# Kernel tuning notes

Measured on AMD Instinct MI355X. Metric: run time of the kernel, lower is better.

## Reference

```python
import jax, jax.numpy as jnp
import numpy as np

N_NODES = 50000
N_EDGES = 800000
IN_FEATS = 128
N_HIDDEN = 64
OUT_FEATS = 40
DIM = 8  # pseudo-coordinate dimension
K = 1    # n_kernels


def setup_inputs() -> dict:
    key = jax.random.key(0)
    ks = jax.random.split(key, 12)
    inp = {
        "features": jax.random.normal(ks[0], (N_NODES, IN_FEATS), dtype=jnp.float32),
        "edge_weight": jax.random.normal(ks[1], (N_EDGES, DIM), dtype=jnp.float32),
        "src": jax.random.randint(ks[2], (N_EDGES,), 0, N_NODES),
        "dst": jax.random.randint(ks[3], (N_EDGES,), 0, N_NODES),
        # layer 1 params (fc has no bias in DGL GMMConv; separate additive bias)
        "W1": jax.random.normal(ks[4], (IN_FEATS, K * N_HIDDEN), dtype=jnp.float32) * (1.0 / np.sqrt(IN_FEATS)),
        "b1": jnp.zeros((N_HIDDEN,), dtype=jnp.float32),
        "mu1": jax.random.normal(ks[5], (K, DIM), dtype=jnp.float32) * 0.1,
        "inv_sigma1": jnp.ones((K, DIM), dtype=jnp.float32),
        # layer 2 params
        "W2": jax.random.normal(ks[6], (N_HIDDEN, K * OUT_FEATS), dtype=jnp.float32) * (1.0 / np.sqrt(N_HIDDEN)),
        "b2": jnp.zeros((OUT_FEATS,), dtype=jnp.float32),
        "mu2": jax.random.normal(ks[7], (K, DIM), dtype=jnp.float32) * 0.1,
        "inv_sigma2": jnp.ones((K, DIM), dtype=jnp.float32),
    }
    return inp


def gmm_conv(x, pseudo, src, dst, W, b, mu, inv_sigma, out_feats):
    # x: [N, in], pseudo: [E, DIM], W: [in, K*out]
    h = (x @ W).reshape(-1, K, out_feats)                      # [N, K, out]
    # gaussian mixture weights per edge/kernel: [E, K]
    diff = pseudo[:, None, :] - mu[None, :, :]                 # [E, K, DIM]
    gw = jnp.exp(-0.5 * jnp.sum(diff * diff * (inv_sigma[None] ** 2), axis=-1))
    # gather src feats, weight, sum over kernels: [E, out]
    msg = jnp.einsum("ekf,ek->ef", h[src], gw)
    agg = jax.ops.segment_sum(msg, dst, num_segments=N_NODES)  # [N, out]
    return agg + b


def reference(features, edge_weight, src, dst, W1, b1, mu1, inv_sigma1, W2, b2, mu2, inv_sigma2):
    x = gmm_conv(features, edge_weight, src, dst, W1, b1, mu1, inv_sigma1, N_HIDDEN)
    x = gmm_conv(x, edge_weight, src, dst, W2, b2, mu2, inv_sigma2, OUT_FEATS)
    return jax.nn.log_softmax(x, axis=1)
```

## Files before the change

### kernel.cpp

```cpp
#include <hip/hip_runtime.h>
#include <hip/hip_fp16.h>
#include <math.h>

#define N_NODES 50000
#define N_EDGES 800000
#define IN_FEATS 128
#define N_HIDDEN 64
#define OUT_FEATS 40
#define DIM 8
#define GT_TILES ((N_NODES + 63) / 64)
#define FILL_BLOCKS (N_EDGES / 256)
#define SCAN_NB ((N_NODES + 255) / 256)

typedef _Float16 half8 __attribute__((ext_vector_type(8)));
typedef float floatx4 __attribute__((ext_vector_type(4)));

__device__ __forceinline__ int wave_incl_scan(int x, int lane) {
#pragma unroll
    for (int off = 1; off < 64; off <<= 1) {
        int v = __shfl_up(x, off, 64);
        if (lane >= off) x += v;
    }
    return x;
}

__global__ __launch_bounds__(256) void hist_kernel(const int* __restrict__ dst,
                                                   int* __restrict__ counts,
                                                   unsigned short* __restrict__ rank) {
    int i = blockIdx.x * 256 + threadIdx.x;
    if (i * 4 >= N_EDGES) return;
    int4 d = ((const int4*)dst)[i];
    ushort4 r;
    r.x = (unsigned short)atomicAdd(&counts[d.x], 1);
    r.y = (unsigned short)atomicAdd(&counts[d.y], 1);
    r.z = (unsigned short)atomicAdd(&counts[d.z], 1);
    r.w = (unsigned short)atomicAdd(&counts[d.w], 1);
    ((ushort4*)rank)[i] = r;
}

__global__ __launch_bounds__(256) void scan_partial_kernel(const int* __restrict__ counts,
                                                           int* __restrict__ offsets,
                                                           int* __restrict__ partials) {
    const int tid = threadIdx.x, bid = blockIdx.x;
    const int i = bid * 256 + tid;
    const int lane = tid & 63, wid = tid >> 6;
    int x = (i < N_NODES) ? counts[i] : 0;
    int incl = wave_incl_scan(x, lane);
    __shared__ int wsum[4];
    if (lane == 63) wsum[wid] = incl;
    __syncthreads();
    int base = 0;
#pragma unroll
    for (int w = 0; w < 4; ++w)
        if (w < wid) base += wsum[w];
    if (i < N_NODES) offsets[i] = base + incl - x;
    if (tid == 255) partials[bid] = base + incl;
}

__global__ __launch_bounds__(256) void scan_base_kernel(int* __restrict__ partials) {
    const int tid = threadIdx.x;
    const int lane = tid & 63, wid = tid >> 6;
    int x = (tid < SCAN_NB) ? partials[tid] : 0;
    int incl = wave_incl_scan(x, lane);
    __shared__ int wsum[4];
    if (lane == 63) wsum[wid] = incl;
    __syncthreads();
    int base = 0;
#pragma unroll
    for (int w = 0; w < 4; ++w)
        if (w < wid) base += wsum[w];
    if (tid < SCAN_NB) partials[tid] = base + incl - x;
}

__global__ __launch_bounds__(256) void scan_add_kernel(int* __restrict__ offsets,
                                                       const int* __restrict__ partials) {
    const int i = blockIdx.x * 256 + threadIdx.x;
    if (i < N_NODES) offsets[i] += partials[blockIdx.x];
    if (i == N_NODES) offsets[N_NODES] = N_EDGES;
}

__global__ __launch_bounds__(256) void fillgemm_kernel(
    const float* __restrict__ features, const float* __restrict__ W1,
    const int* __restrict__ src, const int* __restrict__ dst,
    const float* __restrict__ ew,
    const float* __restrict__ mu1, const float* __restrict__ is1,
    const float* __restrict__ mu2, const float* __restrict__ is2,
    const int* __restrict__ offsets, const unsigned short* __restrict__ rank,
    int2* __restrict__ csr, __half* __restrict__ h1)
{
    const int tid = threadIdx.x;
    __shared__ __align__(16) __half WT[64][136];

    if (blockIdx.x >= GT_TILES) {
        int e = (blockIdx.x - GT_TILES) * 256 + tid;
        int sN = src[e];
        int dN = dst[e];
        unsigned short rk = rank[e];
        const float4* ew4 = (const float4*)(ew + (size_t)e * DIM);
        float4 wa = ew4[0], wb = ew4[1];
        float v[8] = {wa.x, wa.y, wa.z, wa.w, wb.x, wb.y, wb.z, wb.w};
        float s1 = 0.f, s2 = 0.f;
#pragma unroll
        for (int d = 0; d < DIM; ++d) {
            float d1 = v[d] - mu1[d]; float a1 = is1[d];
            float d2 = v[d] - mu2[d]; float a2 = is2[d];
            s1 += d1 * d1 * a1 * a1;
            s2 += d2 * d2 * a2 * a2;
        }
        __half2 g = __floats2half2_rn(expf(-0.5f * s1), expf(-0.5f * s2));
        int2 rec;
        rec.x = sN;
        rec.y = *reinterpret_cast<int*>(&g);
        int pos = offsets[dN] + rk;
        __builtin_nontemporal_store(*reinterpret_cast<long long*>(&rec),
                                    reinterpret_cast<long long*>(&csr[pos]));
        return;
    }

    int nodeBase = blockIdx.x * 64;
    for (int rep = 0; rep < 32; ++rep) {
        int idx = tid + rep * 256;
        int k = idx >> 6, n = idx & 63;
        WT[n][k] = __float2half(W1[idx]);
    }
    __syncthreads();

    int lane = tid & 63, w = tid >> 6;
    int m = lane & 15, quad = lane >> 4;
    int row = nodeBase + w * 16 + m;
    int rowc = (row < N_NODES) ? row : (N_NODES - 1);
    const float* fr = features + (size_t)rowc * IN_FEATS;

    floatx4 acc0 = {0.f,0.f,0.f,0.f}, acc1 = acc0, acc2 = acc0, acc3 = acc0;
#pragma unroll
    for (int kc = 0; kc < 4; ++kc) {
        float4 fa = *(const float4*)(fr + kc * 32 + quad * 8);
        float4 fb = *(const float4*)(fr + kc * 32 + quad * 8 + 4);
        union { half8 v; __half2 h2[4]; } A;
        A.h2[0] = __floats2half2_rn(fa.x, fa.y);
        A.h2[1] = __floats2half2_rn(fa.z, fa.w);
        A.h2[2] = __floats2half2_rn(fb.x, fb.y);
        A.h2[3] = __floats2half2_rn(fb.z, fb.w);
        half8 b0 = *(const half8*)&WT[ 0 + m][kc * 32 + quad * 8];
        half8 b1 = *(const half8*)&WT[16 + m][kc * 32 + quad * 8];
        half8 b2 = *(const half8*)&WT[32 + m][kc * 32 + quad * 8];
        half8 b3 = *(const half8*)&WT[48 + m][kc * 32 + quad * 8];
        acc0 = __builtin_amdgcn_mfma_f32_16x16x32_f16(A.v, b0, acc0, 0, 0, 0);
        acc1 = __builtin_amdgcn_mfma_f32_16x16x32_f16(A.v, b1, acc1, 0, 0, 0);
        acc2 = __builtin_amdgcn_mfma_f32_16x16x32_f16(A.v, b2, acc2, 0, 0, 0);
        acc3 = __builtin_amdgcn_mfma_f32_16x16x32_f16(A.v, b3, acc3, 0, 0, 0);
    }
    int nodeRow = nodeBase + w * 16 + quad * 4;
#pragma unroll
    for (int r = 0; r < 4; ++r) {
        int n = nodeRow + r;
        if (n < N_NODES) {
            size_t base = (size_t)n * N_HIDDEN + m;
            h1[base +  0] = __float2half(acc0[r]);
            h1[base + 16] = __float2half(acc1[r]);
            h1[base + 32] = __float2half(acc2[r]);
            h1[base + 48] = __float2half(acc3[r]);
        }
    }
}

__global__ __launch_bounds__(256) void agg1_gemm2_kernel(const __half* __restrict__ h,
                                                         const int* __restrict__ offsets,
                                                         const int2* __restrict__ csr,
                                                         const float* __restrict__ b,
                                                         const float* __restrict__ W2,
                                                         __half* __restrict__ h2) {
    __shared__ float xs[8][64];
    const unsigned* h32 = (const unsigned*)h;
    const int tid = threadIdx.x;
    const int w = tid >> 6, lane = tid & 63;
    const int hf = lane >> 5, p = lane & 31;
    const int ln = w * 2 + hf;
    const int n = blockIdx.x * 8 + ln;
    int beg = offsets[n], end = offsets[n + 1];

    float ax = 0.f, ay = 0.f;
    for (int j = beg; j < end; j += 8) {
        int j0 = j + 0, j1 = j + 1, j2 = j + 2, j3 = j + 3;
        int j4 = j + 4, j5 = j + 5, j6 = j + 6, j7 = j + 7;
        int e1 = end - 1;
        int2 r0 = csr[(j0 < end) ? j0 : e1];
        int2 r1 = csr[(j1 < end) ? j1 : e1];
        int2 r2 = csr[(j2 < end) ? j2 : e1];
        int2 r3 = csr[(j3 < end) ? j3 : e1];
        int2 r4 = csr[(j4 < end) ? j4 : e1];
        int2 r5 = csr[(j5 < end) ? j5 : e1];
        int2 r6 = csr[(j6 < end) ? j6 : e1];
        int2 r7 = csr[(j7 < end) ? j7 : e1];
        unsigned v0 = h32[(size_t)r0.x * 32 + p];
        unsigned v1 = h32[(size_t)r1.x * 32 + p];
        unsigned v2 = h32[(size_t)r2.x * 32 + p];
        unsigned v3 = h32[(size_t)r3.x * 32 + p];
        unsigned v4 = h32[(size_t)r4.x * 32 + p];
        unsigned v5 = h32[(size_t)r5.x * 32 + p];
        unsigned v6 = h32[(size_t)r6.x * 32 + p];
        unsigned v7 = h32[(size_t)r7.x * 32 + p];
        float g0 = (j0 < end) ? __low2float(*reinterpret_cast<__half2*>(&r0.y)) : 0.f;
        float g1 = (j1 < end) ? __low2float(*reinterpret_cast<__half2*>(&r1.y)) : 0.f;
        float g2 = (j2 < end) ? __low2float(*reinterpret_cast<__half2*>(&r2.y)) : 0.f;
        float g3 = (j3 < end) ? __low2float(*reinterpret_cast<__half2*>(&r3.y)) : 0.f;
        float g4 = (j4 < end) ? __low2float(*reinterpret_cast<__half2*>(&r4.y)) : 0.f;
        float g5 = (j5 < end) ? __low2float(*reinterpret_cast<__half2*>(&r5.y)) : 0.f;
        float g6 = (j6 < end) ? __low2float(*reinterpret_cast<__half2*>(&r6.y)) : 0.f;
        float g7 = (j7 < end) ? __low2float(*reinterpret_cast<__half2*>(&r7.y)) : 0.f;
        float2 f0 = __half22float2(*reinterpret_cast<__half2*>(&v0));
        float2 f1 = __half22float2(*reinterpret_cast<__half2*>(&v1));
        float2 f2 = __half22float2(*reinterpret_cast<__half2*>(&v2));
        float2 f3 = __half22float2(*reinterpret_cast<__half2*>(&v3));
        float2 f4 = __half22float2(*reinterpret_cast<__half2*>(&v4));
        float2 f5 = __half22float2(*reinterpret_cast<__half2*>(&v5));
        float2 f6 = __half22float2(*reinterpret_cast<__half2*>(&v6));
        float2 f7 = __half22float2(*reinterpret_cast<__half2*>(&v7));
        ax += f0.x * g0; ay += f0.y * g0;
        ax += f1.x * g1; ay += f1.y * g1;
        ax += f2.x * g2; ay += f2.y * g2;
        ax += f3.x * g3; ay += f3.y * g3;
        ax += f4.x * g4; ay += f4.y * g4;
        ax += f5.x * g5; ay += f5.y * g5;
        ax += f6.x * g6; ay += f6.y * g6;
        ax += f7.x * g7; ay += f7.y * g7;
    }
    float2 bb = *(const float2*)&b[2 * p];
    *(float2*)&xs[ln][2 * p] = make_float2(ax + bb.x, ay + bb.y);
    __syncthreads();

    for (int o = tid; o < 8 * OUT_FEATS; o += 256) {
        int node = o / OUT_FEATS, t = o % OUT_FEATS;
        const float* xr = xs[node];
        float acc = 0.f;
#pragma unroll
        for (int k = 0; k < N_HIDDEN; ++k)
            acc += xr[k] * W2[k * OUT_FEATS + t];
        h2[(size_t)(blockIdx.x * 8 + node) * OUT_FEATS + t] = __float2half(acc);
    }
}

__global__ __launch_bounds__(256) void agg2_kernel(const __half* __restrict__ h,
                                                   const int* __restrict__ offsets,
                                                   const int2* __restrict__ csr,
                                                   const float* __restrict__ b,
                                                   float* __restrict__ out) {
    const unsigned* h32 = (const unsigned*)h;
    const int tid = threadIdx.x;
    const int w = tid >> 6, lane = tid & 63;
    const int hf = lane >> 5, p = lane & 31;
    const int n = blockIdx.x * 8 + w * 2 + hf;
    const int pc = (p < 20) ? p : 19;
    int beg = offsets[n], end = offsets[n + 1];

    float ax = 0.f, ay = 0.f;
    for (int j = beg; j < end; j += 8) {
        int j0 = j + 0, j1 = j + 1, j2 = j + 2, j3 = j + 3;
        int j4 = j + 4, j5 = j + 5, j6 = j + 6, j7 = j + 7;
        int e1 = end - 1;
        int2 r0 = csr[(j0 < end) ? j0 : e1];
        int2 r1 = csr[(j1 < end) ? j1 : e1];
        int2 r2 = csr[(j2 < end) ? j2 : e1];
        int2 r3 = csr[(j3 < end) ? j3 : e1];
        int2 r4 = csr[(j4 < end) ? j4 : e1];
        int2 r5 = csr[(j5 < end) ? j5 : e1];
        int2 r6 = csr[(j6 < end) ? j6 : e1];
        int2 r7 = csr[(j7 < end) ? j7 : e1];
        unsigned v0 = h32[(size_t)r0.x * 20 + pc];
        unsigned v1 = h32[(size_t)r1.x * 20 + pc];
        unsigned v2 = h32[(size_t)r2.x * 20 + pc];
        unsigned v3 = h32[(size_t)r3.x * 20 + pc];
        unsigned v4 = h32[(size_t)r4.x * 20 + pc];
        unsigned v5 = h32[(size_t)r5.x * 20 + pc];
        unsigned v6 = h32[(size_t)r6.x * 20 + pc];
        unsigned v7 = h32[(size_t)r7.x * 20 + pc];
        float g0 = (j0 < end) ? __high2float(*reinterpret_cast<__half2*>(&r0.y)) : 0.f;
        float g1 = (j1 < end) ? __high2float(*reinterpret_cast<__half2*>(&r1.y)) : 0.f;
        float g2 = (j2 < end) ? __high2float(*reinterpret_cast<__half2*>(&r2.y)) : 0.f;
        float g3 = (j3 < end) ? __high2float(*reinterpret_cast<__half2*>(&r3.y)) : 0.f;
        float g4 = (j4 < end) ? __high2float(*reinterpret_cast<__half2*>(&r4.y)) : 0.f;
        float g5 = (j5 < end) ? __high2float(*reinterpret_cast<__half2*>(&r5.y)) : 0.f;
        float g6 = (j6 < end) ? __high2float(*reinterpret_cast<__half2*>(&r6.y)) : 0.f;
        float g7 = (j7 < end) ? __high2float(*reinterpret_cast<__half2*>(&r7.y)) : 0.f;
        float2 f0 = __half22float2(*reinterpret_cast<__half2*>(&v0));
        float2 f1 = __half22float2(*reinterpret_cast<__half2*>(&v1));
        float2 f2 = __half22float2(*reinterpret_cast<__half2*>(&v2));
        float2 f3 = __half22float2(*reinterpret_cast<__half2*>(&v3));
        float2 f4 = __half22float2(*reinterpret_cast<__half2*>(&v4));
        float2 f5 = __half22float2(*reinterpret_cast<__half2*>(&v5));
        float2 f6 = __half22float2(*reinterpret_cast<__half2*>(&v6));
        float2 f7 = __half22float2(*reinterpret_cast<__half2*>(&v7));
        ax += f0.x * g0; ay += f0.y * g0;
        ax += f1.x * g1; ay += f1.y * g1;
        ax += f2.x * g2; ay += f2.y * g2;
        ax += f3.x * g3; ay += f3.y * g3;
        ax += f4.x * g4; ay += f4.y * g4;
        ax += f5.x * g5; ay += f5.y * g5;
        ax += f6.x * g6; ay += f6.y * g6;
        ax += f7.x * g7; ay += f7.y * g7;
    }

    bool valid = (p < 20);
    float vx = valid ? ax + b[2 * p]     : -INFINITY;
    float vy = valid ? ay + b[2 * p + 1] : -INFINITY;
    float m = fmaxf(vx, vy);
#pragma unroll
    for (int off = 16; off; off >>= 1)
        m = fmaxf(m, __shfl_xor(m, off, 32));
    float ex = valid ? (expf(vx - m) + expf(vy - m)) : 0.f;
#pragma unroll
    for (int off = 16; off; off >>= 1)
        ex += __shfl_xor(ex, off, 32);
    float ls = logf(ex);
    if (valid) {
        float2 o = make_float2(vx - m - ls, vy - m - ls);
        *(float2*)&out[(size_t)n * OUT_FEATS + 2 * p] = o;
    }
}

extern "C" void kernel_launch(void* const* d_in, const int* in_sizes, int n_in,
                              void* d_out, int out_size, void* d_ws, size_t ws_size,
                              hipStream_t stream) {
    const float* features    = (const float*)d_in[0];
    const float* edge_weight = (const float*)d_in[1];
    const int*   src         = (const int*)d_in[2];
    const int*   dst         = (const int*)d_in[3];
    const float* W1          = (const float*)d_in[4];
    const float* b1          = (const float*)d_in[5];
    const float* mu1         = (const float*)d_in[6];
    const float* is1         = (const float*)d_in[7];
    const float* W2          = (const float*)d_in[8];
    const float* b2          = (const float*)d_in[9];
    const float* mu2         = (const float*)d_in[10];
    const float* is2         = (const float*)d_in[11];
    float* out = (float*)d_out;

    int2*           csr     = (int2*)d_ws;
    __half*         h1      = (__half*)(csr + N_EDGES);
    __half*         h2      = h1 + (size_t)N_NODES * N_HIDDEN;
    int*            counts  = (int*)(h2 + (size_t)N_NODES * OUT_FEATS);
    unsigned short* rank    = (unsigned short*)(counts + N_NODES);
    int*            offsets = (int*)(rank + N_EDGES);
    int*            partials= offsets + N_NODES + 1;

    hipMemsetAsync(counts, 0, N_NODES * sizeof(int), stream);

    hist_kernel<<<(N_EDGES / 4 + 255) / 256, 256, 0, stream>>>(dst, counts, rank);

    scan_partial_kernel<<<SCAN_NB, 256, 0, stream>>>(counts, offsets, partials);
    scan_base_kernel<<<1, 256, 0, stream>>>(partials);
    scan_add_kernel<<<SCAN_NB, 256, 0, stream>>>(offsets, partials);

    fillgemm_kernel<<<GT_TILES + FILL_BLOCKS, 256, 0, stream>>>(
        features, W1, src, dst, edge_weight, mu1, is1, mu2, is2, offsets, rank, csr, h1);

    agg1_gemm2_kernel<<<N_NODES / 8, 256, 0, stream>>>(h1, offsets, csr, b1, W2, h2);

    agg2_kernel<<<N_NODES / 8, 256, 0, stream>>>(h2, offsets, csr, b2, out);
}
```

Before: 238.7 us.

## Fuse histogram with first GEMM and pad atomic counters to reduce contention

Moves the GEMM tiles for layer 1 out of the CSR-fill kernel and into the histogram kernel, so the atomic histogram and the GEMM run together in one launch while fill becomes a standalone kernel. The per-node counters are also spaced four ints apart to spread atomics across more cache lines. The goal is to hide the latency-bound atomic pass behind compute-heavy GEMM blocks. The cost is a larger memset and strided scan reads over the counters.

```diff
diff --git a/kernel.cpp b/kernel.cpp
--- a/kernel.cpp
+++ b/kernel.cpp
@@ -9,8 +9,10 @@
 #define OUT_FEATS 40
 #define DIM 8
 #define GT_TILES ((N_NODES + 63) / 64)
+#define HIST_NB ((N_EDGES / 4 + 255) / 256)
 #define FILL_BLOCKS (N_EDGES / 256)
 #define SCAN_NB ((N_NODES + 255) / 256)
+#define CNT_STRIDE 4
 
 typedef _Float16 half8 __attribute__((ext_vector_type(8)));
 typedef float floatx4 __attribute__((ext_vector_type(4)));
@@ -24,100 +26,29 @@
     return x;
 }
 
-__global__ __launch_bounds__(256) void hist_kernel(const int* __restrict__ dst,
-                                                   int* __restrict__ counts,
-                                                   unsigned short* __restrict__ rank) {
-    int i = blockIdx.x * 256 + threadIdx.x;
-    if (i * 4 >= N_EDGES) return;
-    int4 d = ((const int4*)dst)[i];
-    ushort4 r;
-    r.x = (unsigned short)atomicAdd(&counts[d.x], 1);
-    r.y = (unsigned short)atomicAdd(&counts[d.y], 1);
-    r.z = (unsigned short)atomicAdd(&counts[d.z], 1);
-    r.w = (unsigned short)atomicAdd(&counts[d.w], 1);
-    ((ushort4*)rank)[i] = r;
-}
-
-__global__ __launch_bounds__(256) void scan_partial_kernel(const int* __restrict__ counts,
-                                                           int* __restrict__ offsets,
-                                                           int* __restrict__ partials) {
-    const int tid = threadIdx.x, bid = blockIdx.x;
-    const int i = bid * 256 + tid;
-    const int lane = tid & 63, wid = tid >> 6;
-    int x = (i < N_NODES) ? counts[i] : 0;
-    int incl = wave_incl_scan(x, lane);
-    __shared__ int wsum[4];
-    if (lane == 63) wsum[wid] = incl;
-    __syncthreads();
-    int base = 0;
-#pragma unroll
-    for (int w = 0; w < 4; ++w)
-        if (w < wid) base += wsum[w];
-    if (i < N_NODES) offsets[i] = base + incl - x;
-    if (tid == 255) partials[bid] = base + incl;
-}
-
-__global__ __launch_bounds__(256) void scan_base_kernel(int* __restrict__ partials) {
-    const int tid = threadIdx.x;
-    const int lane = tid & 63, wid = tid >> 6;
-    int x = (tid < SCAN_NB) ? partials[tid] : 0;
-    int incl = wave_incl_scan(x, lane);
-    __shared__ int wsum[4];
-    if (lane == 63) wsum[wid] = incl;
-    __syncthreads();
-    int base = 0;
-#pragma unroll
-    for (int w = 0; w < 4; ++w)
-        if (w < wid) base += wsum[w];
-    if (tid < SCAN_NB) partials[tid] = base + incl - x;
-}
-
-__global__ __launch_bounds__(256) void scan_add_kernel(int* __restrict__ offsets,
-                                                       const int* __restrict__ partials) {
-    const int i = blockIdx.x * 256 + threadIdx.x;
-    if (i < N_NODES) offsets[i] += partials[blockIdx.x];
-    if (i == N_NODES) offsets[N_NODES] = N_EDGES;
-}
-
-__global__ __launch_bounds__(256) void fillgemm_kernel(
+__global__ __launch_bounds__(256) void histgemm_kernel(
     const float* __restrict__ features, const float* __restrict__ W1,
-    const int* __restrict__ src, const int* __restrict__ dst,
-    const float* __restrict__ ew,
-    const float* __restrict__ mu1, const float* __restrict__ is1,
-    const float* __restrict__ mu2, const float* __restrict__ is2,
-    const int* __restrict__ offsets, const unsigned short* __restrict__ rank,
-    int2* __restrict__ csr, __half* __restrict__ h1)
+    const int* __restrict__ dst,
+    int* __restrict__ counts, unsigned short* __restrict__ rank,
+    __half* __restrict__ h1)
 {
     const int tid = threadIdx.x;
     __shared__ __align__(16) __half WT[64][136];
 
-    if (blockIdx.x >= GT_TILES) {
-        int e = (blockIdx.x - GT_TILES) * 256 + tid;
-        int sN = src[e];
-        int dN = dst[e];
-        unsigned short rk = rank[e];
-        const float4* ew4 = (const float4*)(ew + (size_t)e * DIM);
-        float4 wa = ew4[0], wb = ew4[1];
-        float v[8] = {wa.x, wa.y, wa.z, wa.w, wb.x, wb.y, wb.z, wb.w};
-        float s1 = 0.f, s2 = 0.f;
-#pragma unroll
-        for (int d = 0; d < DIM; ++d) {
-            float d1 = v[d] - mu1[d]; float a1 = is1[d];
-            float d2 = v[d] - mu2[d]; float a2 = is2[d];
-            s1 += d1 * d1 * a1 * a1;
-            s2 += d2 * d2 * a2 * a2;
-        }
-        __half2 g = __floats2half2_rn(expf(-0.5f * s1), expf(-0.5f * s2));
-        int2 rec;
-        rec.x = sN;
-        rec.y = *reinterpret_cast<int*>(&g);
-        int pos = offsets[dN] + rk;
-        __builtin_nontemporal_store(*reinterpret_cast<long long*>(&rec),
-                                    reinterpret_cast<long long*>(&csr[pos]));
+    if (blockIdx.x < HIST_NB) {
+        int i = blockIdx.x * 256 + tid;
+        if (i * 4 >= N_EDGES) return;
+        int4 d = ((const int4*)dst)[i];
+        ushort4 r;
+        r.x = (unsigned short)atomicAdd(&counts[d.x * CNT_STRIDE], 1);
+        r.y = (unsigned short)atomicAdd(&counts[d.y * CNT_STRIDE], 1);
+        r.z = (unsigned short)atomicAdd(&counts[d.z * CNT_STRIDE], 1);
+        r.w = (unsigned short)atomicAdd(&counts[d.w * CNT_STRIDE], 1);
+        ((ushort4*)rank)[i] = r;
         return;
     }
 
-    int nodeBase = blockIdx.x * 64;
+    int nodeBase = (blockIdx.x - HIST_NB) * 64;
     for (int rep = 0; rep < 32; ++rep) {
         int idx = tid + rep * 256;
         int k = idx >> 6, n = idx & 63;
@@ -162,6 +93,79 @@
             h1[base + 48] = __float2half(acc3[r]);
         }
     }
+}
+
+__global__ __launch_bounds__(256) void scan_partial_kernel(const int* __restrict__ counts,
+                                                           int* __restrict__ offsets,
+                                                           int* __restrict__ partials) {
+    const int tid = threadIdx.x, bid = blockIdx.x;
+    const int i = bid * 256 + tid;
+    const int lane = tid & 63, wid = tid >> 6;
+    int x = (i < N_NODES) ? counts[i * CNT_STRIDE] : 0;
+    int incl = wave_incl_scan(x, lane);
+    __shared__ int wsum[4];
+    if (lane == 63) wsum[wid] = incl;
+    __syncthreads();
+    int base = 0;
+#pragma unroll
+    for (int w = 0; w < 4; ++w)
+        if (w < wid) base += wsum[w];
+    if (i < N_NODES) offsets[i] = base + incl - x;
+    if (tid == 255) partials[bid] = base + incl;
+}
+
+__global__ __launch_bounds__(256) void scan_base_kernel(int* __restrict__ partials) {
+    const int tid = threadIdx.x;
+    const int lane = tid & 63, wid = tid >> 6;
+    int x = (tid < SCAN_NB) ? partials[tid] : 0;
+    int incl = wave_incl_scan(x, lane);
+    __shared__ int wsum[4];
+    if (lane == 63) wsum[wid] = incl;
+    __syncthreads();
+    int base = 0;
+#pragma unroll
+    for (int w = 0; w < 4; ++w)
+        if (w < wid) base += wsum[w];
+    if (tid < SCAN_NB) partials[tid] = base + incl - x;
+}
+
+__global__ __launch_bounds__(256) void scan_add_kernel(int* __restrict__ offsets,
+                                                       const int* __restrict__ partials) {
+    const int i = blockIdx.x * 256 + threadIdx.x;
+    if (i < N_NODES) offsets[i] += partials[blockIdx.x];
+    if (i == N_NODES) offsets[N_NODES] = N_EDGES;
+}
+
+__global__ __launch_bounds__(256) void fill_kernel(
+    const int* __restrict__ src, const int* __restrict__ dst,
+    const float* __restrict__ ew,
+    const float* __restrict__ mu1, const float* __restrict__ is1,
+    const float* __restrict__ mu2, const float* __restrict__ is2,
+    const int* __restrict__ offsets, const unsigned short* __restrict__ rank,
+    int2* __restrict__ csr)
+{
+    int e = blockIdx.x * 256 + threadIdx.x;
+    int sN = src[e];
+    int dN = dst[e];
+    unsigned short rk = rank[e];
+    const float4* ew4 = (const float4*)(ew + (size_t)e * DIM);
+    float4 wa = ew4[0], wb = ew4[1];
+    float v[8] = {wa.x, wa.y, wa.z, wa.w, wb.x, wb.y, wb.z, wb.w};
+    float s1 = 0.f, s2 = 0.f;
+#pragma unroll
+    for (int d = 0; d < DIM; ++d) {
+        float d1 = v[d] - mu1[d]; float a1 = is1[d];
+        float d2 = v[d] - mu2[d]; float a2 = is2[d];
+        s1 += d1 * d1 * a1 * a1;
+        s2 += d2 * d2 * a2 * a2;
+    }
+    __half2 g = __floats2half2_rn(expf(-0.5f * s1), expf(-0.5f * s2));
+    int2 rec;
+    rec.x = sN;
+    rec.y = *reinterpret_cast<int*>(&g);
+    int pos = offsets[dN] + rk;
+    __builtin_nontemporal_store(*reinterpret_cast<long long*>(&rec),
+                                reinterpret_cast<long long*>(&csr[pos]));
 }
 
 __global__ __launch_bounds__(256) void agg1_gemm2_kernel(const __half* __restrict__ h,
@@ -339,20 +343,21 @@
     __half*         h1      = (__half*)(csr + N_EDGES);
     __half*         h2      = h1 + (size_t)N_NODES * N_HIDDEN;
     int*            counts  = (int*)(h2 + (size_t)N_NODES * OUT_FEATS);
-    unsigned short* rank    = (unsigned short*)(counts + N_NODES);
+    unsigned short* rank    = (unsigned short*)(counts + N_NODES * CNT_STRIDE);
     int*            offsets = (int*)(rank + N_EDGES);
     int*            partials= offsets + N_NODES + 1;
 
-    hipMemsetAsync(counts, 0, N_NODES * sizeof(int), stream);
-
-    hist_kernel<<<(N_EDGES / 4 + 255) / 256, 256, 0, stream>>>(dst, counts, rank);
+    hipMemsetAsync(counts, 0, (size_t)N_NODES * CNT_STRIDE * sizeof(int), stream);
+
+    histgemm_kernel<<<HIST_NB + GT_TILES, 256, 0, stream>>>(
+        features, W1, dst, counts, rank, h1);
 
     scan_partial_kernel<<<SCAN_NB, 256, 0, stream>>>(counts, offsets, partials);
     scan_base_kernel<<<1, 256, 0, stream>>>(partials);
     scan_add_kernel<<<SCAN_NB, 256, 0, stream>>>(offsets, partials);
 
-    fillgemm_kernel<<<GT_TILES + FILL_BLOCKS, 256, 0, stream>>>(
-        features, W1, src, dst, edge_weight, mu1, is1, mu2, is2, offsets, rank, csr, h1);
+    fill_kernel<<<FILL_BLOCKS, 256, 0, stream>>>(
+        src, dst, edge_weight, mu1, is1, mu2, is2, offsets, rank, csr);
 
     agg1_gemm2_kernel<<<N_NODES / 8, 256, 0, stream>>>(h1, offsets, csr, b1, W2, h2);
 
```

Result: no change. 237.8 us (-0.4%).
